# Kernel tuning notes

Measured on AMD Instinct MI355X. Metric: run time of the kernel, lower is better.

Reference implementation:

```python
import jax, jax.numpy as jnp
import numpy as np

NUM_HEADS = 8
N_MOD = 3


def _sinusoidal_pe(seq_len, d_model):
    # standard sinusoidal table [seq_len, d_model]
    pos = np.arange(seq_len, dtype=np.float32)[:, None]
    div = np.exp(np.arange(0, d_model, 2, dtype=np.float32) * (-np.log(10000.0) / d_model))
    pe = np.zeros((seq_len, d_model), dtype=np.float32)
    pe[:, 0::2] = np.sin(pos * div)
    pe[:, 1::2] = np.cos(pos * div)
    return jnp.asarray(pe)


def _attn_mask(dim_x, dim_z, n_mod):
    # additive mask [dim_x, dim_x + n_mod*dim_z]: 0 where allowed, -inf elsewhere
    blocks = [np.eye(dim_x, dtype=np.float32)]
    for _ in range(n_mod):  # all modalities present (mod_list == full_mod)
        p2 = np.zeros((dim_x, dim_z), dtype=np.float32)
        p2[dim_x - dim_z:, :] = np.eye(dim_z, dtype=np.float32)
        blocks.append(p2)
    m = np.concatenate(blocks, axis=1)
    return jnp.asarray(np.where(m < 1, -np.inf, 0.0).astype(np.float32))


def setup_inputs() -> dict:
    key = jax.random.key(0)
    ks = jax.random.split(key, 8)
    bs, en, dx, dz = 32, 256, 512, 256
    state = jax.random.normal(ks[0], (bs, en, dx), jnp.float32)
    obs0 = jax.random.normal(ks[1], (bs, en, dz), jnp.float32)
    obs1 = jax.random.normal(ks[2], (bs, en, dz), jnp.float32)
    obs2 = jax.random.normal(ks[3], (bs, en, dz), jnp.float32)
    Q = jax.random.uniform(ks[4], (dx, en), jnp.float32)  # torch.rand init
    Wq = jax.random.normal(ks[5], (en, en), jnp.float32) / np.sqrt(en)
    Wk = jax.random.normal(ks[6], (en, en), jnp.float32) / np.sqrt(en)
    bq = jnp.zeros((en,), jnp.float32)
    bk = jnp.zeros((en,), jnp.float32)
    return {"state": state, "obs0": obs0, "obs1": obs1, "obs2": obs2,
            "Q": Q, "Wq": Wq, "bq": bq, "Wk": Wk, "bk": bk}


def reference(state, obs0, obs1, obs2, Q, Wq, bq, Wk, bk):
    bs, en, dx = state.shape
    dz = obs0.shape[2]
    obs_list = (obs0, obs1, obs2)
    mask = _attn_mask(dx, dz, N_MOD)            # [dx, L]
    pe = _sinusoidal_pe(bs, en)                 # positions run over batch axis (faithful quirk)

    # mean-center over the ensemble axis
    A = state - jnp.mean(state, axis=1, keepdims=True)          # [bs, en, dx]
    Ys = [o - jnp.mean(o, axis=1, keepdims=True) for o in obs_list]

    # build query / key-value sequences in [tokens, bs, en] layout, add PE, then batch-major
    q = Q[:, None, :] + pe[None, :, :]                          # [dx, bs, en]
    xy = jnp.concatenate([jnp.transpose(A, (2, 0, 1))]
                         + [jnp.transpose(Y, (2, 0, 1)) for Y in Ys], axis=0)
    xy = xy + pe[None, :, :]                                    # [L, bs, en]
    qb = jnp.transpose(q, (1, 0, 2))                            # [bs, dx, en]
    kb = jnp.transpose(xy, (1, 0, 2))                           # [bs, L, en]

    # multi-head masked attention (output path is discarded by the original module,
    # only the attention map is used, so no V/O projection is needed)
    dh = en // NUM_HEADS
    qh = (qb @ Wq + bq).reshape(bs, dx, NUM_HEADS, dh).transpose(0, 2, 1, 3)   # [bs,h,dx,dh]
    kh = (kb @ Wk + bk).reshape(bs, -1, NUM_HEADS, dh).transpose(0, 2, 1, 3)   # [bs,h,L,dh]
    scores = jnp.einsum('bhqd,bhkd->bhqk', qh, kh) / np.sqrt(dh).astype(np.float32)
    scores = scores + mask[None, None, :, :]
    atten = jnp.mean(jax.nn.softmax(scores, axis=-1), axis=1)   # [bs, dx, L]

    # attn-weighted matmul over concatenated raw state+obs
    merge = jnp.concatenate([state, obs0, obs1, obs2], axis=2)  # [bs, en, L]
    new_state = jnp.einsum('bql,bel->beq', atten, merge)        # [bs, en, dx]
    return new_state, atten
```

## Files before the change

### kernel.cpp

```cpp
#include <hip/hip_runtime.h>
#include <math.h>


__global__ __launch_bounds__(256)
void k_uv_copy(const float* __restrict__ Q, const float* __restrict__ Wq,
               const float* __restrict__ bq, const float* __restrict__ state,
               float* __restrict__ uT, float* __restrict__ vT,
               float* __restrict__ out0) {
  const int blk = blockIdx.x;
  const int t = threadIdx.x;
  if (blk < 288) {
    __shared__ float row[256];
    float rv;
    if (blk < 256) {
      rv = Q[(256 + blk) * 256 + t];
    } else {
      const int b = blk - 256;
      const float dv = expf(-9.210340371976184f * (float)((t >> 1) << 1) * (1.0f / 256.0f));
      const float ang = (float)b * dv;
      rv = (t & 1) ? cosf(ang) : sinf(ang);
    }
    row[t] = rv;
    __syncthreads();
    float acc = (blk < 256) ? 0.0f : bq[t];
    for (int e = 0; e < 256; ++e) acc += row[e] * Wq[e * 256 + t];
    if (blk < 256) uT[t * 256 + blk] = acc;
    else           vT[t * 32 + (blk - 256)] = acc;
  } else {
    const int id = blk - 288;
    const int b = id >> 5, eg = id & 31;
    const int r = t >> 5;
    const int c = t & 31;
    const int e = eg * 8 + r;
    const size_t base = ((size_t)(b * 256 + e)) * 512;
    *(float4*)(out0 + base + c * 4)        = *(const float4*)(state + base + c * 4);
    *(float4*)(out0 + base + (c + 32) * 4) = *(const float4*)(state + base + (c + 32) * 4);
  }
}

__global__ __launch_bounds__(256)
void k_w_onehot(const float* __restrict__ Wk, const float* __restrict__ uT,
                const float* __restrict__ vT, float* __restrict__ wu2,
                float* __restrict__ wv, float* __restrict__ out1) {
  const int blk = blockIdx.x;
  const int t = threadIdx.x;
  if (blk < 512) {
    const int e = blk & 255;
    const int part = blk >> 8;
    __shared__ float wrow[256];
    wrow[t] = Wk[e * 256 + t];
    __syncthreads();
    if (part == 0) {
#pragma unroll
      for (int h = 0; h < 8; ++h) {
        float acc = 0.0f;
#pragma unroll
        for (int d = 0; d < 32; ++d)
          acc += uT[(h * 32 + d) * 256 + t] * wrow[h * 32 + d];
        wu2[(size_t)(h * 256 + e) * 272 + t] = acc;
      }
    } else if (t < 32) {
#pragma unroll
      for (int h = 0; h < 8; ++h) {
        float acc = 0.0f;
#pragma unroll
        for (int d = 0; d < 32; ++d)
          acc += vT[(h * 32 + d) * 32 + t] * wrow[h * 32 + d];
        wv[(t * 8 + h) * 256 + e] = acc;
      }
    }
  } else {
    const int id = blk - 512;
    const int b = id >> 5, qg = id & 31;
#pragma unroll
    for (int k = 0; k < 8; ++k) {
      const int q = qg * 8 + k;
      float4* row = (float4*)(out1 + ((size_t)(b * 512 + q)) * 1280);
      float4 o = make_float4(0.f, 0.f, 0.f, 0.f);
      if (t == (q >> 2)) {
        const int comp = q & 3;
        if (comp == 0) o.x = 1.f; else if (comp == 1) o.y = 1.f;
        else if (comp == 2) o.z = 1.f; else o.w = 1.f;
      }
      row[t] = o;
      if (t < 64) row[256 + t] = make_float4(0.f, 0.f, 0.f, 0.f);
    }
  }
}

__global__ __launch_bounds__(512)
void k_all(const float* __restrict__ state, const float* __restrict__ o0,
           const float* __restrict__ o1, const float* __restrict__ o2,
           const float* __restrict__ wu2, const float* __restrict__ wv,
           float* __restrict__ out0, float* __restrict__ out1) {
  const int t = threadIdx.x;
  const int jt = blockIdx.x;
  const int b  = blockIdx.y;

  __shared__ float s_data[4][128][17];
  __shared__ float s_wvb[2048];
  __shared__ float s_part[8][16][25];
  __shared__ float s_tot[44][16];
  __shared__ float s_a[16][4];

  for (int i = t; i < 2048; i += 512) s_wvb[i] = wv[b * 2048 + i];

  const int jl = t & 15;
  const int es = (t >> 4) & 15;
  const int hp = t >> 8;
  const int j = jt * 16 + jl;

  float acc[24];
#pragma unroll
  for (int k = 0; k < 24; ++k) acc[k] = 0.f;

  const float* pwu = wu2 + (size_t)hp * 4 * 256 * 272 + j;
  const float* pwvb = s_wvb + hp * 4 * 256;

#pragma unroll
  for (int chunk = 0; chunk < 2; ++chunk) {
    __syncthreads();
#pragma unroll
    for (int rep = 0; rep < 4; ++rep) {
      const int c = t + rep * 512;
      const int m = c >> 9;
      const int r = c & 511;
      const int e = r >> 2;
      const int jq = r & 3;
      const int ge = chunk * 128 + e;
      const int j0 = jt * 16 + jq * 4;
      const float* src;
      if (m == 0)      src = state + ((size_t)(b * 256 + ge)) * 512 + 256 + j0;
      else if (m == 1) src = o0 + ((size_t)(b * 256 + ge)) * 256 + j0;
      else if (m == 2) src = o1 + ((size_t)(b * 256 + ge)) * 256 + j0;
      else             src = o2 + ((size_t)(b * 256 + ge)) * 256 + j0;
      const float4 v4 = *(const float4*)src;
      const int jb = jq * 4;
      s_data[m][e][jb]   = v4.x; s_data[m][e][jb+1] = v4.y;
      s_data[m][e][jb+2] = v4.z; s_data[m][e][jb+3] = v4.w;
    }
    __syncthreads();

#pragma unroll
    for (int it = 0; it < 8; ++it) {
      const int el = it * 16 + es;
      const int e = chunk * 128 + el;
      const float s  = s_data[0][el][jl];
      const float x0 = s_data[1][el][jl];
      const float x1 = s_data[2][el][jl];
      const float x2 = s_data[3][el][jl];
      acc[20] += s; acc[21] += x0; acc[22] += x1; acc[23] += x2;
#pragma unroll
      for (int hh = 0; hh < 4; ++hh) {
        const float w = pwu[(size_t)(hh * 256 + e) * 272] + pwvb[hh * 256 + e];
        acc[hh * 5 + 0] += s * w;  acc[hh * 5 + 1] += x0 * w;
        acc[hh * 5 + 2] += x1 * w; acc[hh * 5 + 3] += x2 * w;
        acc[hh * 5 + 4] += w;
      }
    }
  }

#pragma unroll
  for (int k = 0; k < 24; ++k) {
    acc[k] += __shfl_xor(acc[k], 16);
    acc[k] += __shfl_xor(acc[k], 32);
  }
  if ((t & 48) == 0) {
    const int w = t >> 6;
    float* p = &s_part[w][jl][0];
#pragma unroll
    for (int k = 0; k < 24; ++k) p[k] = acc[k];
  }
  __syncthreads();

  if (t < 16) {
#pragma unroll
    for (int k = 0; k < 20; ++k)
      s_tot[k][t] = s_part[0][t][k] + s_part[1][t][k] + s_part[2][t][k] + s_part[3][t][k];
#pragma unroll
    for (int c = 0; c < 4; ++c)
      s_tot[40 + c][t] = s_part[0][t][20 + c] + s_part[1][t][20 + c] +
                         s_part[2][t][20 + c] + s_part[3][t][20 + c];
  } else if (t >= 256 && t < 272) {
    const int l = t & 15;
#pragma unroll
    for (int k = 0; k < 20; ++k)
      s_tot[20 + k][l] = s_part[4][l][k] + s_part[5][l][k] + s_part[6][l][k] + s_part[7][l][k];
  }
  __syncthreads();

  if (t < 16) {
    float tot[44];
#pragma unroll
    for (int k = 0; k < 44; ++k) tot[k] = s_tot[k][t];
    const float m0 = tot[40] * (1.f / 256.f), m1 = tot[41] * (1.f / 256.f);
    const float m2 = tot[42] * (1.f / 256.f), m3 = tot[43] * (1.f / 256.f);
    const float inv = 0.17677669529663687f;
    float am0 = 0.f, am1 = 0.f, am2 = 0.f, am3 = 0.f;
#pragma unroll
    for (int h = 0; h < 8; ++h) {
      const float dO = tot[h * 5 + 4];
      const float s0 = (tot[h * 5 + 0] - m0 * dO) * inv;
      const float s1 = (tot[h * 5 + 1] - m1 * dO) * inv;
      const float s2 = (tot[h * 5 + 2] - m2 * dO) * inv;
      const float s3 = (tot[h * 5 + 3] - m3 * dO) * inv;
      const float mx = fmaxf(fmaxf(s0, s1), fmaxf(s2, s3));
      const float e0 = expf(s0 - mx), e1 = expf(s1 - mx);
      const float e2 = expf(s2 - mx), e3 = expf(s3 - mx);
      const float r = 1.f / (e0 + e1 + e2 + e3);
      am0 += e0 * r; am1 += e1 * r; am2 += e2 * r; am3 += e3 * r;
    }
    s_a[t][0] = am0 * 0.125f; s_a[t][1] = am1 * 0.125f;
    s_a[t][2] = am2 * 0.125f; s_a[t][3] = am3 * 0.125f;
  }
  __syncthreads();

  {
    const int jl2 = t & 15;
    const int er = t >> 4;
    const float a0 = s_a[jl2][0], a1 = s_a[jl2][1];
    const float a2 = s_a[jl2][2], a3 = s_a[jl2][3];
    const int jj = jt * 16 + jl2;
#pragma unroll
    for (int k = 0; k < 4; ++k) {
      const int e = er + 32 * k;
      const size_t idxS = ((size_t)(b * 256 + e)) * 512 + 256 + jj;
      const size_t idxO = ((size_t)(b * 256 + e)) * 256 + jj;
      out0[idxS] = a0 * state[idxS] + a1 * o0[idxO] + a2 * o1[idxO] + a3 * o2[idxO];
    }
#pragma unroll
    for (int k = 4; k < 8; ++k) {
      const int e = er + 32 * k;
      const int el = e - 128;
      const size_t idxS = ((size_t)(b * 256 + e)) * 512 + 256 + jj;
      out0[idxS] = a0 * s_data[0][el][jl2] + a1 * s_data[1][el][jl2] +
                   a2 * s_data[2][el][jl2] + a3 * s_data[3][el][jl2];
    }
  }

  {
    const int r = t >> 5;
    const int c = t & 31;
    const int j3 = jt * 16 + r;
    const int q = 256 + j3;
    const int comp = j3 & 3;
    const int tc0 = (256 + j3) >> 2, tc1 = (512 + j3) >> 2;
    const int tc2 = (768 + j3) >> 2, tc3 = (1024 + j3) >> 2;
    const float av0 = s_a[r][0], av1 = s_a[r][1];
    const float av2 = s_a[r][2], av3 = s_a[r][3];
    float4* orow = (float4*)(out1 + ((size_t)(b * 512 + q)) * 1280);
#pragma unroll
    for (int k = 0; k < 10; ++k) {
      const int c4 = c + 32 * k;
      float4 o = make_float4(0.f, 0.f, 0.f, 0.f);
      float val = 0.f; bool hit = false;
      if (c4 == tc0)      { val = av0; hit = true; }
      else if (c4 == tc1) { val = av1; hit = true; }
      else if (c4 == tc2) { val = av2; hit = true; }
      else if (c4 == tc3) { val = av3; hit = true; }
      if (hit) {
        if (comp == 0) o.x = val; else if (comp == 1) o.y = val;
        else if (comp == 2) o.z = val; else o.w = val;
      }
      orow[c4] = o;
    }
  }
}

extern "C" void kernel_launch(void* const* d_in, const int* in_sizes, int n_in,
                              void* d_out, int out_size, void* d_ws, size_t ws_size,
                              hipStream_t stream) {
  const float* state = (const float*)d_in[0];
  const float* obs0  = (const float*)d_in[1];
  const float* obs1  = (const float*)d_in[2];
  const float* obs2  = (const float*)d_in[3];
  const float* Q     = (const float*)d_in[4];
  const float* Wq    = (const float*)d_in[5];
  const float* bq    = (const float*)d_in[6];
  const float* Wk    = (const float*)d_in[7];

  float* out0 = (float*)d_out;
  float* out1 = out0 + (size_t)32 * 256 * 512;

  float* ws  = (float*)d_ws;
  float* uT  = ws;
  float* vT  = uT + 65536;
  float* wu2 = vT + 8192;
  float* wv  = wu2 + 557056;

  k_uv_copy<<<1312, 256, 0, stream>>>(Q, Wq, bq, state, uT, vT, out0);
  k_w_onehot<<<1536, 256, 0, stream>>>(Wk, uT, vT, wu2, wv, out1);
  k_all<<<dim3(16, 32), 512, 0, stream>>>(state, obs0, obs1, obs2, wu2, wv, out0, out1);
}
```

Before: 60.47 us.

## Register-prefetch next input chunk and alternate chunk order across blocks

The staged load of state/obs tiles is split into four 64-row stages, and the next stage is prefetched into registers while the current one is reduced from LDS. Blocks with odd (jt^b) walk the stages in reverse, which staggers the order in which neighbouring blocks touch global memory. The final output pass reads the last two stages still resident in LDS, wherever they sit, instead of always assuming the upper half. This trades extra registers and one more barrier pair per stage for latency hiding, and the reversed order may reduce L2/channel contention.

```diff
diff --git a/kernel.cpp b/kernel.cpp
--- a/kernel.cpp
+++ b/kernel.cpp
@@ -96,6 +96,7 @@
   const int t = threadIdx.x;
   const int jt = blockIdx.x;
   const int b  = blockIdx.y;
+  const int corder = (jt ^ b) & 1;
 
   __shared__ float s_data[4][128][17];
   __shared__ float s_wvb[2048];
@@ -110,6 +111,13 @@
   const int hp = t >> 8;
   const int j = jt * 16 + jl;
 
+  const int mA = t >> 8;
+  const int rA = t & 255;
+  const int eA = rA >> 2;
+  const int jqA = rA & 3;
+  const int mB = mA + 2;
+  const int j0A = jt * 16 + jqA * 4;
+
   float acc[24];
 #pragma unroll
   for (int k = 0; k < 24; ++k) acc[k] = 0.f;
@@ -117,48 +125,57 @@
   const float* pwu = wu2 + (size_t)hp * 4 * 256 * 272 + j;
   const float* pwvb = s_wvb + hp * 4 * 256;
 
-#pragma unroll
-  for (int chunk = 0; chunk < 2; ++chunk) {
+  auto ld = [&](int m, int ge) -> float4 {
+    const float* src;
+    if (m == 0)      src = state + ((size_t)(b * 256 + ge)) * 512 + 256 + j0A;
+    else if (m == 1) src = o0 + ((size_t)(b * 256 + ge)) * 256 + j0A;
+    else if (m == 2) src = o1 + ((size_t)(b * 256 + ge)) * 256 + j0A;
+    else             src = o2 + ((size_t)(b * 256 + ge)) * 256 + j0A;
+    return *(const float4*)src;
+  };
+
+  int s0 = corder ? 3 : 0;
+  float4 regA = ld(mA, s0 * 64 + eA);
+  float4 regB = ld(mB, s0 * 64 + eA);
+
+#pragma unroll
+  for (int ss = 0; ss < 4; ++ss) {
+    const int s = corder ? 3 - ss : ss;
+    const int eb = (s & 1) * 64;
     __syncthreads();
-#pragma unroll
-    for (int rep = 0; rep < 4; ++rep) {
-      const int c = t + rep * 512;
-      const int m = c >> 9;
-      const int r = c & 511;
-      const int e = r >> 2;
-      const int jq = r & 3;
-      const int ge = chunk * 128 + e;
-      const int j0 = jt * 16 + jq * 4;
-      const float* src;
-      if (m == 0)      src = state + ((size_t)(b * 256 + ge)) * 512 + 256 + j0;
-      else if (m == 1) src = o0 + ((size_t)(b * 256 + ge)) * 256 + j0;
-      else if (m == 2) src = o1 + ((size_t)(b * 256 + ge)) * 256 + j0;
-      else             src = o2 + ((size_t)(b * 256 + ge)) * 256 + j0;
-      const float4 v4 = *(const float4*)src;
-      const int jb = jq * 4;
-      s_data[m][e][jb]   = v4.x; s_data[m][e][jb+1] = v4.y;
-      s_data[m][e][jb+2] = v4.z; s_data[m][e][jb+3] = v4.w;
+    {
+      const int jb = jqA * 4;
+      s_data[mA][eb + eA][jb]   = regA.x; s_data[mA][eb + eA][jb+1] = regA.y;
+      s_data[mA][eb + eA][jb+2] = regA.z; s_data[mA][eb + eA][jb+3] = regA.w;
+      s_data[mB][eb + eA][jb]   = regB.x; s_data[mB][eb + eA][jb+1] = regB.y;
+      s_data[mB][eb + eA][jb+2] = regB.z; s_data[mB][eb + eA][jb+3] = regB.w;
     }
     __syncthreads();
-
-#pragma unroll
-    for (int it = 0; it < 8; ++it) {
+    if (ss < 3) {
+      const int sn = corder ? 3 - (ss + 1) : ss + 1;
+      regA = ld(mA, sn * 64 + eA);
+      regB = ld(mB, sn * 64 + eA);
+    }
+#pragma unroll
+    for (int it = 0; it < 4; ++it) {
       const int el = it * 16 + es;
-      const int e = chunk * 128 + el;
-      const float s  = s_data[0][el][jl];
-      const float x0 = s_data[1][el][jl];
-      const float x1 = s_data[2][el][jl];
-      const float x2 = s_data[3][el][jl];
-      acc[20] += s; acc[21] += x0; acc[22] += x1; acc[23] += x2;
+      const int e = s * 64 + el;
+      const int lr = eb + el;
+      const float sv = s_data[0][lr][jl];
+      const float x0 = s_data[1][lr][jl];
+      const float x1 = s_data[2][lr][jl];
+      const float x2 = s_data[3][lr][jl];
+      acc[20] += sv; acc[21] += x0; acc[22] += x1; acc[23] += x2;
 #pragma unroll
       for (int hh = 0; hh < 4; ++hh) {
         const float w = pwu[(size_t)(hh * 256 + e) * 272] + pwvb[hh * 256 + e];
-        acc[hh * 5 + 0] += s * w;  acc[hh * 5 + 1] += x0 * w;
-        acc[hh * 5 + 2] += x1 * w; acc[hh * 5 + 3] += x2 * w;
+        acc[hh * 5 + 0] += sv * w;  acc[hh * 5 + 1] += x0 * w;
+        acc[hh * 5 + 2] += x1 * w;  acc[hh * 5 + 3] += x2 * w;
         acc[hh * 5 + 4] += w;
       }
     }
   }
+  const int lds_e0 = corder ? 0 : 128;
 
 #pragma unroll
   for (int k = 0; k < 24; ++k) {
@@ -200,13 +217,13 @@
 #pragma unroll
     for (int h = 0; h < 8; ++h) {
       const float dO = tot[h * 5 + 4];
-      const float s0 = (tot[h * 5 + 0] - m0 * dO) * inv;
-      const float s1 = (tot[h * 5 + 1] - m1 * dO) * inv;
-      const float s2 = (tot[h * 5 + 2] - m2 * dO) * inv;
-      const float s3 = (tot[h * 5 + 3] - m3 * dO) * inv;
-      const float mx = fmaxf(fmaxf(s0, s1), fmaxf(s2, s3));
-      const float e0 = expf(s0 - mx), e1 = expf(s1 - mx);
-      const float e2 = expf(s2 - mx), e3 = expf(s3 - mx);
+      const float s0v = (tot[h * 5 + 0] - m0 * dO) * inv;
+      const float s1v = (tot[h * 5 + 1] - m1 * dO) * inv;
+      const float s2v = (tot[h * 5 + 2] - m2 * dO) * inv;
+      const float s3v = (tot[h * 5 + 3] - m3 * dO) * inv;
+      const float mx = fmaxf(fmaxf(s0v, s1v), fmaxf(s2v, s3v));
+      const float e0 = expf(s0v - mx), e1 = expf(s1v - mx);
+      const float e2 = expf(s2v - mx), e3 = expf(s3v - mx);
       const float r = 1.f / (e0 + e1 + e2 + e3);
       am0 += e0 * r; am1 += e1 * r; am2 += e2 * r; am3 += e3 * r;
     }
@@ -222,19 +239,18 @@
     const float a2 = s_a[jl2][2], a3 = s_a[jl2][3];
     const int jj = jt * 16 + jl2;
 #pragma unroll
-    for (int k = 0; k < 4; ++k) {
+    for (int k = 0; k < 8; ++k) {
       const int e = er + 32 * k;
       const size_t idxS = ((size_t)(b * 256 + e)) * 512 + 256 + jj;
-      const size_t idxO = ((size_t)(b * 256 + e)) * 256 + jj;
-      out0[idxS] = a0 * state[idxS] + a1 * o0[idxO] + a2 * o1[idxO] + a3 * o2[idxO];
-    }
-#pragma unroll
-    for (int k = 4; k < 8; ++k) {
-      const int e = er + 32 * k;
-      const int el = e - 128;
-      const size_t idxS = ((size_t)(b * 256 + e)) * 512 + 256 + jj;
-      out0[idxS] = a0 * s_data[0][el][jl2] + a1 * s_data[1][el][jl2] +
-                   a2 * s_data[2][el][jl2] + a3 * s_data[3][el][jl2];
+      const bool in_lds = (e >= lds_e0) && (e < lds_e0 + 128);
+      if (in_lds) {
+        const int el = e - lds_e0;
+        out0[idxS] = a0 * s_data[0][el][jl2] + a1 * s_data[1][el][jl2] +
+                     a2 * s_data[2][el][jl2] + a3 * s_data[3][el][jl2];
+      } else {
+        const size_t idxO = ((size_t)(b * 256 + e)) * 256 + jj;
+        out0[idxS] = a0 * state[idxS] + a1 * o0[idxO] + a2 * o1[idxO] + a3 * o2[idxO];
+      }
     }
   }
 
```

Measured after the change: 60.02 us. No clear change (-0.7%).
